# Optimization experiments

Measured on AMD Instinct MI355X. Metric: run time of the kernel, lower is better.

Reference implementation:

```python
import jax, jax.numpy as jnp
import numpy as np

B, N, F_IN = 8, 2048, 16
E, H = 64, 4
D = E // H
HID, A = 128, 4
QUEUE_IDX = np.array([0, 1, 2, 3, 6, 7, 8, 9, 10, 11, 12, 13])


def setup_inputs() -> dict:
    key = jax.random.key(0)
    ks = iter(jax.random.split(key, 64))
    def g(*s, scale=0.05):
        return jax.random.normal(next(ks), s, jnp.float32) * scale
    inp = {}
    inp['node_features'] = jax.random.normal(next(ks), (B, N, F_IN), jnp.float32) * 10.0
    inp['adjacency'] = jax.random.randint(next(ks), (B, N, N), 0, 2).astype(jnp.float32)
    for i, fin in enumerate([F_IN, E]):
        inp[f'l{i}_wq'] = g(fin, E)
        inp[f'l{i}_wk'] = g(fin, E)
        inp[f'l{i}_wv'] = g(fin, E)
        inp[f'l{i}_in_w'] = g(E, 3 * E)
        inp[f'l{i}_in_b'] = jnp.zeros(3 * E, jnp.float32)
        inp[f'l{i}_mha_ow'] = g(E, E)
        inp[f'l{i}_mha_ob'] = jnp.zeros(E, jnp.float32)
        inp[f'l{i}_op_w'] = g(E, E)
        inp[f'l{i}_op_b'] = jnp.zeros(E, jnp.float32)
    inp['head_w1'] = g(E, HID)
    inp['head_b1'] = jnp.zeros(HID, jnp.float32)
    inp['head_w2'] = g(HID, HID)
    inp['head_b2'] = jnp.zeros(HID, jnp.float32)
    inp['head_w3'] = g(HID, A, scale=0.001)
    inp['head_b3'] = jnp.zeros(A, jnp.float32)
    return inp


def _gat_layer(x, mask, wq, wk, wv, in_w, in_b, mow, mob, opw, opb):
    # x: [B,N,Fin], mask: [B,N,N] bool (True = blocked)
    b, n, _ = x.shape
    q = x @ wq  # layer's own Q/K/V projections (bias-free)
    k = x @ wk
    v = x @ wv
    # nn.MultiheadAttention's internal in_proj (with bias)
    Q = q @ in_w[:, :E] + in_b[:E]
    K = k @ in_w[:, E:2 * E] + in_b[E:2 * E]
    V = v @ in_w[:, 2 * E:] + in_b[2 * E:]
    Qh = Q.reshape(b, n, H, D)
    Kh = K.reshape(b, n, H, D)
    Vh = V.reshape(b, n, H, D)
    s = jnp.einsum('bqhd,bkhd->bhqk', Qh, Kh) / jnp.sqrt(jnp.float32(D))
    s = jnp.where(mask[:, None, :, :], -jnp.inf, s)
    a = jax.nn.softmax(s, axis=-1)  # diagonal always unmasked -> no all-inf rows
    o = jnp.einsum('bhqk,bkhd->bqhd', a, Vh).reshape(b, n, E)
    o = o @ mow + mob  # MHA out_proj
    return o @ opw + opb  # layer out_proj


def reference(node_features, adjacency,
              l0_wq, l0_wk, l0_wv, l0_in_w, l0_in_b, l0_mha_ow, l0_mha_ob, l0_op_w, l0_op_b,
              l1_wq, l1_wk, l1_wv, l1_in_w, l1_in_b, l1_mha_ow, l1_mha_ob, l1_op_w, l1_op_b,
              head_w1, head_b1, head_w2, head_b2, head_w3, head_b3):
    f = node_features.shape[-1]
    scale = jnp.ones(f, node_features.dtype).at[QUEUE_IDX].set(1.0 / 50.0).at[5].set(1.0 / 300.0)
    x = node_features * scale
    n = adjacency.shape[-1]
    mask = (adjacency + jnp.eye(n, dtype=adjacency.dtype)) == 0
    x = jax.nn.relu(_gat_layer(x, mask, l0_wq, l0_wk, l0_wv, l0_in_w, l0_in_b, l0_mha_ow, l0_mha_ob, l0_op_w, l0_op_b))
    x = jax.nn.relu(_gat_layer(x, mask, l1_wq, l1_wk, l1_wv, l1_in_w, l1_in_b, l1_mha_ow, l1_mha_ob, l1_op_w, l1_op_b))
    h = jax.nn.relu(x @ head_w1 + head_b1)
    h = jax.nn.relu(h @ head_w2 + head_b2)
    return h @ head_w3 + head_b3  # [B, N, n_actions]
```

## Files before the change

kernel.cpp:

```cpp
#include <hip/hip_runtime.h>

#define BB 8
#define NN 2048
#define FIN0 16
#define EE 64
#define HH 4
#define DD 16
#define HIDN 128
#define AA 4

__global__ __launch_bounds__(256) void k_mask(const float* __restrict__ adj, unsigned long long* __restrict__ mbT) {
    const int ITER = 32;
    for (int it = 0; it < ITER; it++) {
        long long idx = ((long long)blockIdx.x * ITER + it) * 256 + threadIdx.x;
        int k = (int)(idx & (NN - 1));
        int r = (int)((idx >> 11) & (NN - 1));
        int b = (int)(idx >> 22);
        float a = adj[idx];
        bool blocked = (a == 0.0f) && (k != r);
        unsigned long long m = __ballot(blocked);
        if ((threadIdx.x & 63) == 0) mbT[((long long)b * 32 + (k >> 6)) * NN + r] = m;
    }
}

#define QSCALE 0.36067376022224085f
__device__ __forceinline__ float sfeat(int f) {
    return (f == 4 || f == 14 || f == 15) ? 1.0f : ((f == 5) ? (1.0f / 300.0f) : 0.02f);
}
__global__ __launch_bounds__(256) void k_wcomb(
        const float* __restrict__ wq0, const float* __restrict__ wk0, const float* __restrict__ wv0,
        const float* __restrict__ inw0, const float* __restrict__ inb0,
        const float* __restrict__ mow0, const float* __restrict__ mob0,
        const float* __restrict__ opw0, const float* __restrict__ opb0,
        const float* __restrict__ wq1, const float* __restrict__ wk1, const float* __restrict__ wv1,
        const float* __restrict__ inw1, const float* __restrict__ inb1,
        const float* __restrict__ mow1, const float* __restrict__ mob1,
        const float* __restrict__ opw1, const float* __restrict__ opb1,
        float* __restrict__ CW0, float* __restrict__ WO0, float* __restrict__ bO0, float* __restrict__ bQ0,
        float* __restrict__ CW1, float* __restrict__ WO1, float* __restrict__ bO1, float* __restrict__ bQ1) {
    int ly = blockIdx.y;
    int fin = ly ? EE : FIN0;
    const float* wq = ly ? wq1 : wq0; const float* wk = ly ? wk1 : wk0; const float* wv = ly ? wv1 : wv0;
    const float* inw = ly ? inw1 : inw0; const float* inb = ly ? inb1 : inb0;
    const float* mow = ly ? mow1 : mow0; const float* mob = ly ? mob1 : mob0;
    const float* opw = ly ? opw1 : opw0; const float* opb = ly ? opb1 : opb0;
    float* CW = ly ? CW1 : CW0; float* WO = ly ? WO1 : WO0;
    float* bO = ly ? bO1 : bO0; float* bQ = ly ? bQ1 : bQ0;

    int t = blockIdx.x * 256 + threadIdx.x;
    int t1 = fin * 192;
    int t2 = t1 + 4096;
    int t3 = t2 + 64;
    int t4 = t3 + 192;
    if (t < t1) {
        int f = t / 192, j = t % 192;
        const float* w = (j < 64) ? wq : ((j < 128) ? wk : wv);
        float acc = 0.f;
        for (int kk = 0; kk < 64; kk++) acc += w[f * 64 + kk] * inw[kk * 192 + j];
        if (j < 64) acc *= QSCALE;
        if (ly == 0) acc *= sfeat(f);
        CW[t] = acc;
    } else if (t < t2) {
        int u = t - t1; int i = u >> 6, j = u & 63;
        float acc = 0.f;
        for (int kk = 0; kk < 64; kk++) acc += mow[i * 64 + kk] * opw[kk * 64 + j];
        WO[u] = acc;
    } else if (t < t3) {
        int j = t - t2;
        float acc = opb[j];
        for (int kk = 0; kk < 64; kk++) acc += mob[kk] * opw[kk * 64 + j];
        bO[j] = acc;
    } else if (t < t4) {
        int j = t - t3;
        bQ[j] = inb[j] * ((j < 64) ? QSCALE : 1.0f);
    }
}

template <int FINP>
__global__ __launch_bounds__(256) void k_qkv(const float* __restrict__ X, const float* __restrict__ CW,
                                             const float* __restrict__ bQ,
                                             float* __restrict__ Q, float* __restrict__ K, float* __restrict__ V) {
    int lane = threadIdx.x & 63;
    int quarter = threadIdx.x >> 6;
    int row = blockIdx.x * 64 + lane;
    int b = row >> 11, n = row & (NN - 1);
    float xr[FINP];
    const float4* xp = (const float4*)(X + (long long)row * FINP);
#pragma unroll
    for (int i = 0; i < FINP / 4; i++) {
        float4 v = xp[i];
        xr[4 * i] = v.x; xr[4 * i + 1] = v.y; xr[4 * i + 2] = v.z; xr[4 * i + 3] = v.w;
    }
    for (int jq = 0; jq < 12; jq++) {
        int j = quarter * 48 + jq * 4;
        float4 acc = *(const float4*)(bQ + j);
#pragma unroll
        for (int f = 0; f < FINP; f++) {
            float4 w = *(const float4*)(CW + f * 192 + j);
            acc.x = fmaf(xr[f], w.x, acc.x);
            acc.y = fmaf(xr[f], w.y, acc.y);
            acc.z = fmaf(xr[f], w.z, acc.z);
            acc.w = fmaf(xr[f], w.w, acc.w);
        }
        int which = j >> 6, c = j & 63, h = c >> 4, d = c & 15;
        float* dst = (which == 0) ? Q : ((which == 1) ? K : V);
        *(float4*)(dst + (((long long)(b * HH + h) * NN + n) * DD + d)) = acc;
    }
}

__global__ __launch_bounds__(256) void k_attn(const float* __restrict__ Q, const float* __restrict__ K,
                                              const float* __restrict__ V,
                                              const unsigned long long* __restrict__ mbT,
                                              float* __restrict__ O) {
    __shared__ __align__(16) float smem[2 * 4 * 64 * 17];
    int lane = threadIdx.x & 63;
    int w = threadIdx.x >> 6;
    int qb = blockIdx.x, h = blockIdx.y, b = blockIdx.z;
    int q0 = qb * 128 + lane;
    const float* Qp0 = Q + ((long long)((b * HH + h) * NN) + q0) * DD;
    const float4* qv0 = (const float4*)Qp0;
    const float4* qv1 = (const float4*)(Qp0 + 64 * DD);
    float4 q00 = qv0[0], q01 = qv0[1], q02 = qv0[2], q03 = qv0[3];
    float4 q10 = qv1[0], q11 = qv1[1], q12 = qv1[2], q13 = qv1[3];
    const float* Kb = K + (long long)(b * HH + h) * NN * DD;
    const float* Vb = V + (long long)(b * HH + h) * NN * DD;
    const unsigned long long* mrow = mbT + (long long)b * 32 * NN;
    float4 o00 = {0,0,0,0}, o01 = {0,0,0,0}, o02 = {0,0,0,0}, o03 = {0,0,0,0};
    float4 o10 = {0,0,0,0}, o11 = {0,0,0,0}, o12 = {0,0,0,0}, o13 = {0,0,0,0};
    float l0 = 0.f, l1 = 0.f;
    float* sK = smem + w * 2048;
    float* sV = sK + 1024;
    for (int c = 0; c < 8; c++) {
        int kc = w * 512 + c * 64;
        __syncthreads();
        const float4* srcK = (const float4*)(Kb + (long long)kc * DD);
        const float4* srcV = (const float4*)(Vb + (long long)kc * DD);
#pragma unroll
        for (int i = 0; i < 4; i++) {
            ((float4*)sK)[lane + 64 * i] = srcK[lane + 64 * i];
            ((float4*)sV)[lane + 64 * i] = srcV[lane + 64 * i];
        }
        unsigned long long mw0 = mrow[(long long)(kc >> 6) * NN + q0];
        unsigned long long mw1 = mrow[(long long)(kc >> 6) * NN + q0 + 64];
        __syncthreads();
#pragma unroll 4
        for (int kk = 0; kk < 64; kk++) {
            const float4* kr = (const float4*)(sK + kk * 16);
            float4 k0 = kr[0], k1 = kr[1], k2 = kr[2], k3 = kr[3];
            float cA = q00.x * k0.x;
            cA = fmaf(q00.y, k0.y, cA); cA = fmaf(q00.z, k0.z, cA); cA = fmaf(q00.w, k0.w, cA);
            cA = fmaf(q01.x, k1.x, cA); cA = fmaf(q01.y, k1.y, cA); cA = fmaf(q01.z, k1.z, cA); cA = fmaf(q01.w, k1.w, cA);
            float cB = q02.x * k2.x;
            cB = fmaf(q02.y, k2.y, cB); cB = fmaf(q02.z, k2.z, cB); cB = fmaf(q02.w, k2.w, cB);
            cB = fmaf(q03.x, k3.x, cB); cB = fmaf(q03.y, k3.y, cB); cB = fmaf(q03.w, k3.w, cB); cB = fmaf(q03.z, k3.z, cB);
            float cC = q10.x * k0.x;
            cC = fmaf(q10.y, k0.y, cC); cC = fmaf(q10.z, k0.z, cC); cC = fmaf(q10.w, k0.w, cC);
            cC = fmaf(q11.x, k1.x, cC); cC = fmaf(q11.y, k1.y, cC); cC = fmaf(q11.z, k1.z, cC); cC = fmaf(q11.w, k1.w, cC);
            float cD = q12.x * k2.x;
            cD = fmaf(q12.y, k2.y, cD); cD = fmaf(q12.z, k2.z, cD); cD = fmaf(q12.w, k2.w, cD);
            cD = fmaf(q13.x, k3.x, cD); cD = fmaf(q13.y, k3.y, cD); cD = fmaf(q13.z, k3.z, cD); cD = fmaf(q13.w, k3.w, cD);
            float e0 = __builtin_amdgcn_exp2f(cA + cB);
            float e1 = __builtin_amdgcn_exp2f(cC + cD);
            if ((mw0 >> kk) & 1ULL) e0 = 0.f;
            if ((mw1 >> kk) & 1ULL) e1 = 0.f;
            l0 += e0; l1 += e1;
            const float4* vr = (const float4*)(sV + kk * 16);
            float4 v0 = vr[0], v1 = vr[1], v2 = vr[2], v3 = vr[3];
            o00.x = fmaf(e0, v0.x, o00.x); o00.y = fmaf(e0, v0.y, o00.y); o00.z = fmaf(e0, v0.z, o00.z); o00.w = fmaf(e0, v0.w, o00.w);
            o01.x = fmaf(e0, v1.x, o01.x); o01.y = fmaf(e0, v1.y, o01.y); o01.z = fmaf(e0, v1.z, o01.z); o01.w = fmaf(e0, v1.w, o01.w);
            o02.x = fmaf(e0, v2.x, o02.x); o02.y = fmaf(e0, v2.y, o02.y); o02.z = fmaf(e0, v2.z, o02.z); o02.w = fmaf(e0, v2.w, o02.w);
            o03.x = fmaf(e0, v3.x, o03.x); o03.y = fmaf(e0, v3.y, o03.y); o03.z = fmaf(e0, v3.z, o03.z); o03.w = fmaf(e0, v3.w, o03.w);
            o10.x = fmaf(e1, v0.x, o10.x); o10.y = fmaf(e1, v0.y, o10.y); o10.z = fmaf(e1, v0.z, o10.z); o10.w = fmaf(e1, v0.w, o10.w);
            o11.x = fmaf(e1, v1.x, o11.x); o11.y = fmaf(e1, v1.y, o11.y); o11.z = fmaf(e1, v1.z, o11.z); o11.w = fmaf(e1, v1.w, o11.w);
            o12.x = fmaf(e1, v2.x, o12.x); o12.y = fmaf(e1, v2.y, o12.y); o12.z = fmaf(e1, v2.z, o12.z); o12.w = fmaf(e1, v2.w, o12.w);
            o13.x = fmaf(e1, v3.x, o13.x); o13.y = fmaf(e1, v3.y, o13.y); o13.z = fmaf(e1, v3.z, o13.z); o13.w = fmaf(e1, v3.w, o13.w);
        }
    }
    __syncthreads();
    {
        float* r0 = smem + (((0 * 4 + w) * 64 + lane)) * 17;
        r0[0]=o00.x; r0[1]=o00.y; r0[2]=o00.z; r0[3]=o00.w;
        r0[4]=o01.x; r0[5]=o01.y; r0[6]=o01.z; r0[7]=o01.w;
        r0[8]=o02.x; r0[9]=o02.y; r0[10]=o02.z; r0[11]=o02.w;
        r0[12]=o03.x; r0[13]=o03.y; r0[14]=o03.z; r0[15]=o03.w;
        r0[16]=l0;
        float* r1 = smem + (((1 * 4 + w) * 64 + lane)) * 17;
        r1[0]=o10.x; r1[1]=o10.y; r1[2]=o10.z; r1[3]=o10.w;
        r1[4]=o11.x; r1[5]=o11.y; r1[6]=o11.z; r1[7]=o11.w;
        r1[8]=o12.x; r1[9]=o12.y; r1[10]=o12.z; r1[11]=o12.w;
        r1[12]=o13.x; r1[13]=o13.y; r1[14]=o13.z; r1[15]=o13.w;
        r1[16]=l1;
    }
    __syncthreads();
    if (w < 2) {
        const float* basep = smem + ((w * 4) * 64 + lane) * 17;
        float acc[DD]; float lt = 0.f;
#pragma unroll
        for (int d = 0; d < DD; d++) acc[d] = 0.f;
#pragma unroll
        for (int s2 = 0; s2 < 4; s2++) {
            const float* pp = basep + s2 * 64 * 17;
#pragma unroll
            for (int d = 0; d < DD; d++) acc[d] += pp[d];
            lt += pp[16];
        }
        float inv = 1.0f / lt;
        int q = qb * 128 + w * 64 + lane;
        float* op = O + (long long)(b * NN + q) * EE + h * DD;
        float4 r0 = {acc[0]*inv, acc[1]*inv, acc[2]*inv, acc[3]*inv};
        float4 r1 = {acc[4]*inv, acc[5]*inv, acc[6]*inv, acc[7]*inv};
        float4 r2 = {acc[8]*inv, acc[9]*inv, acc[10]*inv, acc[11]*inv};
        float4 r3 = {acc[12]*inv, acc[13]*inv, acc[14]*inv, acc[15]*inv};
        ((float4*)op)[0] = r0; ((float4*)op)[1] = r1; ((float4*)op)[2] = r2; ((float4*)op)[3] = r3;
    }
}

__global__ __launch_bounds__(256) void k_out(const float* __restrict__ X, const float* __restrict__ WO,
                                             const float* __restrict__ bO, float* __restrict__ Y) {
    int lane = threadIdx.x & 63, quarter = threadIdx.x >> 6;
    long long row = (long long)blockIdx.x * 64 + lane;
    float xr[64];
    const float4* xp = (const float4*)(X + row * 64);
#pragma unroll
    for (int i = 0; i < 16; i++) {
        float4 t = xp[i];
        xr[4 * i] = t.x; xr[4 * i + 1] = t.y; xr[4 * i + 2] = t.z; xr[4 * i + 3] = t.w;
    }
    for (int jq = 0; jq < 4; jq++) {
        int j = quarter * 16 + jq * 4;
        float4 acc = *(const float4*)(bO + j);
#pragma unroll
        for (int f = 0; f < 64; f++) {
            float4 w4 = *(const float4*)(WO + f * 64 + j);
            acc.x = fmaf(xr[f], w4.x, acc.x);
            acc.y = fmaf(xr[f], w4.y, acc.y);
            acc.z = fmaf(xr[f], w4.z, acc.z);
            acc.w = fmaf(xr[f], w4.w, acc.w);
        }
        acc.x = fmaxf(acc.x, 0.f); acc.y = fmaxf(acc.y, 0.f);
        acc.z = fmaxf(acc.z, 0.f); acc.w = fmaxf(acc.w, 0.f);
        *(float4*)(Y + row * 64 + j) = acc;
    }
}

__global__ __launch_bounds__(128) void k_head(const float* __restrict__ X,
                                              const float* __restrict__ w1, const float* __restrict__ b1,
                                              const float* __restrict__ w2, const float* __restrict__ b2,
                                              const float* __restrict__ w3, const float* __restrict__ b3,
                                              float* __restrict__ out) {
    __shared__ float Xs[16 * 64];
    __shared__ float H1[16 * 128];
    __shared__ float H2[16 * 128];
    int tid = threadIdx.x;
    long long row0 = (long long)blockIdx.x * 16;
    {
        const float4* src = (const float4*)(X + row0 * 64);
        float4* dst = (float4*)Xs;
        dst[tid] = src[tid];
        dst[tid + 128] = src[tid + 128];
    }
    __syncthreads();
    {
        float wr[64];
#pragma unroll
        for (int f = 0; f < 64; f++) wr[f] = w1[f * 128 + tid];
        float bb = b1[tid];
        for (int r = 0; r < 16; r++) {
            const float4* x4 = (const float4*)(Xs + r * 64);
            float a0 = bb, a1 = 0.f, a2 = 0.f, a3 = 0.f;
#pragma unroll
            for (int fq = 0; fq < 16; fq++) {
                float4 xv = x4[fq];
                a0 = fmaf(xv.x, wr[4 * fq], a0);
                a1 = fmaf(xv.y, wr[4 * fq + 1], a1);
                a2 = fmaf(xv.z, wr[4 * fq + 2], a2);
                a3 = fmaf(xv.w, wr[4 * fq + 3], a3);
            }
            H1[r * 128 + tid] = fmaxf((a0 + a1) + (a2 + a3), 0.f);
        }
    }
    __syncthreads();
    {
        float wr2[128];
#pragma unroll
        for (int f = 0; f < 128; f++) wr2[f] = w2[f * 128 + tid];
        float bb2 = b2[tid];
        for (int r = 0; r < 16; r++) {
            const float4* h4 = (const float4*)(H1 + r * 128);
            float a0 = bb2, a1 = 0.f, a2 = 0.f, a3 = 0.f;
#pragma unroll
            for (int fq = 0; fq < 32; fq++) {
                float4 xv = h4[fq];
                a0 = fmaf(xv.x, wr2[4 * fq], a0);
                a1 = fmaf(xv.y, wr2[4 * fq + 1], a1);
                a2 = fmaf(xv.z, wr2[4 * fq + 2], a2);
                a3 = fmaf(xv.w, wr2[4 * fq + 3], a3);
            }
            H2[r * 128 + tid] = fmaxf((a0 + a1) + (a2 + a3), 0.f);
        }
    }
    __syncthreads();
    if (tid < 64) {
        int r = tid >> 2, a = tid & 3;
        float acc = b3[a];
        for (int f = 0; f < 128; f++) acc = fmaf(H2[r * 128 + f], w3[f * 4 + a], acc);
        out[(row0 + r) * 4 + a] = acc;
    }
}

extern "C" void kernel_launch(void* const* d_in, const int* in_sizes, int n_in,
                              void* d_out, int out_size, void* d_ws, size_t ws_size,
                              hipStream_t stream) {
    const float* nf = (const float*)d_in[0];
    const float* adj = (const float*)d_in[1];
    const float* l0[9]; for (int i = 0; i < 9; i++) l0[i] = (const float*)d_in[2 + i];
    const float* l1[9]; for (int i = 0; i < 9; i++) l1[i] = (const float*)d_in[11 + i];
    const float* hw1 = (const float*)d_in[20]; const float* hb1 = (const float*)d_in[21];
    const float* hw2 = (const float*)d_in[22]; const float* hb2 = (const float*)d_in[23];
    const float* hw3 = (const float*)d_in[24]; const float* hb3 = (const float*)d_in[25];
    float* out = (float*)d_out;

    char* ws = (char*)d_ws;
    size_t off = 0;
    auto alloc = [&](size_t bytes) -> void* {
        void* p = ws + off;
        off = (off + bytes + 255) & ~(size_t)255;
        return p;
    };
    unsigned long long* mbT = (unsigned long long*)alloc((size_t)BB * NN * NN / 8);
    float* Q = (float*)alloc((size_t)BB * HH * NN * DD * 4);
    float* K = (float*)alloc((size_t)BB * HH * NN * DD * 4);
    float* V = (float*)alloc((size_t)BB * HH * NN * DD * 4);
    float* O = (float*)alloc((size_t)BB * NN * EE * 4);
    float* x1 = (float*)alloc((size_t)BB * NN * EE * 4);
    float* x2 = (float*)alloc((size_t)BB * NN * EE * 4);
    float* CW0 = (float*)alloc(16 * 192 * 4);
    float* CW1 = (float*)alloc(64 * 192 * 4);
    float* WO0 = (float*)alloc(64 * 64 * 4);
    float* WO1 = (float*)alloc(64 * 64 * 4);
    float* bO0 = (float*)alloc(64 * 4);
    float* bO1 = (float*)alloc(64 * 4);
    float* bQ0 = (float*)alloc(192 * 4);
    float* bQ1 = (float*)alloc(192 * 4);

    k_mask<<<4096, 256, 0, stream>>>(adj, mbT);
    k_wcomb<<<dim3(65, 2), 256, 0, stream>>>(
        l0[0], l0[1], l0[2], l0[3], l0[4], l0[5], l0[6], l0[7], l0[8],
        l1[0], l1[1], l1[2], l1[3], l1[4], l1[5], l1[6], l1[7], l1[8],
        CW0, WO0, bO0, bQ0, CW1, WO1, bO1, bQ1);

    k_qkv<16><<<BB * NN / 64, 256, 0, stream>>>(nf, CW0, bQ0, Q, K, V);
    k_attn<<<dim3(NN / 128, HH, BB), 256, 0, stream>>>(Q, K, V, mbT, O);
    k_out<<<BB * NN / 64, 256, 0, stream>>>(O, WO0, bO0, x1);
    k_qkv<64><<<BB * NN / 64, 256, 0, stream>>>(x1, CW1, bQ1, Q, K, V);
    k_attn<<<dim3(NN / 128, HH, BB), 256, 0, stream>>>(Q, K, V, mbT, O);
    k_out<<<BB * NN / 64, 256, 0, stream>>>(O, WO1, bO1, x2);
    k_head<<<BB * NN / 16, 128, 0, stream>>>(x2, hw1, hb1, hw2, hb2, hw3, hb3, out);
}
```

Before: 705.1 us.

## Retile attention to four query rows per lane and fuse out-proj with QKV

The attention kernel now uses 512-thread blocks. Each lane holds four query rows instead of two, so every K/V row read from shared memory feeds twice as many score and accumulate FMAs. Each wave keeps a private K/V staging area, so the per-chunk block barriers are replaced by an LDS waitcnt, and the final reduction now sums eight wave partials. Separately, the layer-0 output projection and the layer-1 QKV projection are fused into one kernel that keeps the intermediate activations in shared memory, which drops a global round-trip and a launch. The risks are higher register pressure, a large shared-memory footprint that limits occupancy to one block per CU, and only 256 attention blocks for the whole grid.

```diff
diff --git a/kernel.cpp b/kernel.cpp
--- a/kernel.cpp
+++ b/kernel.cpp
@@ -108,31 +108,40 @@
     }
 }
 
-__global__ __launch_bounds__(256) void k_attn(const float* __restrict__ Q, const float* __restrict__ K,
-                                              const float* __restrict__ V,
-                                              const unsigned long long* __restrict__ mbT,
-                                              float* __restrict__ O) {
-    __shared__ __align__(16) float smem[2 * 4 * 64 * 17];
+__global__ __launch_bounds__(512, 2) void k_attn(const float* __restrict__ Q, const float* __restrict__ K,
+                                                 const float* __restrict__ V,
+                                                 const unsigned long long* __restrict__ mbT,
+                                                 float* __restrict__ O) {
+    __shared__ float smem[8 * 4 * 64 * 17];
     int lane = threadIdx.x & 63;
     int w = threadIdx.x >> 6;
     int qb = blockIdx.x, h = blockIdx.y, b = blockIdx.z;
-    int q0 = qb * 128 + lane;
-    const float* Qp0 = Q + ((long long)((b * HH + h) * NN) + q0) * DD;
-    const float4* qv0 = (const float4*)Qp0;
-    const float4* qv1 = (const float4*)(Qp0 + 64 * DD);
-    float4 q00 = qv0[0], q01 = qv0[1], q02 = qv0[2], q03 = qv0[3];
-    float4 q10 = qv1[0], q11 = qv1[1], q12 = qv1[2], q13 = qv1[3];
-    const float* Kb = K + (long long)(b * HH + h) * NN * DD;
-    const float* Vb = V + (long long)(b * HH + h) * NN * DD;
+    int qbase = qb * 256;
+
+    const float* Qbh = Q + (long long)(b * HH + h) * NN * DD;
+    const float* Kb  = K + (long long)(b * HH + h) * NN * DD;
+    const float* Vb  = V + (long long)(b * HH + h) * NN * DD;
     const unsigned long long* mrow = mbT + (long long)b * 32 * NN;
-    float4 o00 = {0,0,0,0}, o01 = {0,0,0,0}, o02 = {0,0,0,0}, o03 = {0,0,0,0};
-    float4 o10 = {0,0,0,0}, o11 = {0,0,0,0}, o12 = {0,0,0,0}, o13 = {0,0,0,0};
-    float l0 = 0.f, l1 = 0.f;
+
+    float4 qf[4][4];
+#pragma unroll
+    for (int rq = 0; rq < 4; rq++) {
+        const float4* qp = (const float4*)(Qbh + (long long)(qbase + rq * 64 + lane) * DD);
+#pragma unroll
+        for (int j = 0; j < 4; j++) qf[rq][j] = qp[j];
+    }
+    float4 oacc[4][4];
+#pragma unroll
+    for (int rq = 0; rq < 4; rq++)
+#pragma unroll
+        for (int j = 0; j < 4; j++) oacc[rq][j] = make_float4(0.f, 0.f, 0.f, 0.f);
+    float lsum[4] = {0.f, 0.f, 0.f, 0.f};
+
     float* sK = smem + w * 2048;
     float* sV = sK + 1024;
-    for (int c = 0; c < 8; c++) {
-        int kc = w * 512 + c * 64;
-        __syncthreads();
+
+    for (int c = 0; c < 4; c++) {
+        int kc = w * 256 + c * 64;
         const float4* srcK = (const float4*)(Kb + (long long)kc * DD);
         const float4* srcV = (const float4*)(Vb + (long long)kc * DD);
 #pragma unroll
@@ -140,72 +149,71 @@
             ((float4*)sK)[lane + 64 * i] = srcK[lane + 64 * i];
             ((float4*)sV)[lane + 64 * i] = srcV[lane + 64 * i];
         }
-        unsigned long long mw0 = mrow[(long long)(kc >> 6) * NN + q0];
-        unsigned long long mw1 = mrow[(long long)(kc >> 6) * NN + q0 + 64];
-        __syncthreads();
+        unsigned long long mw[4];
+        int kblk = w * 4 + c;
+#pragma unroll
+        for (int rq = 0; rq < 4; rq++) mw[rq] = mrow[(long long)kblk * NN + qbase + rq * 64 + lane];
+        asm volatile("s_waitcnt lgkmcnt(0)" ::: "memory");
 #pragma unroll 4
         for (int kk = 0; kk < 64; kk++) {
             const float4* kr = (const float4*)(sK + kk * 16);
             float4 k0 = kr[0], k1 = kr[1], k2 = kr[2], k3 = kr[3];
-            float cA = q00.x * k0.x;
-            cA = fmaf(q00.y, k0.y, cA); cA = fmaf(q00.z, k0.z, cA); cA = fmaf(q00.w, k0.w, cA);
-            cA = fmaf(q01.x, k1.x, cA); cA = fmaf(q01.y, k1.y, cA); cA = fmaf(q01.z, k1.z, cA); cA = fmaf(q01.w, k1.w, cA);
-            float cB = q02.x * k2.x;
-            cB = fmaf(q02.y, k2.y, cB); cB = fmaf(q02.z, k2.z, cB); cB = fmaf(q02.w, k2.w, cB);
-            cB = fmaf(q03.x, k3.x, cB); cB = fmaf(q03.y, k3.y, cB); cB = fmaf(q03.w, k3.w, cB); cB = fmaf(q03.z, k3.z, cB);
-            float cC = q10.x * k0.x;
-            cC = fmaf(q10.y, k0.y, cC); cC = fmaf(q10.z, k0.z, cC); cC = fmaf(q10.w, k0.w, cC);
-            cC = fmaf(q11.x, k1.x, cC); cC = fmaf(q11.y, k1.y, cC); cC = fmaf(q11.z, k1.z, cC); cC = fmaf(q11.w, k1.w, cC);
-            float cD = q12.x * k2.x;
-            cD = fmaf(q12.y, k2.y, cD); cD = fmaf(q12.z, k2.z, cD); cD = fmaf(q12.w, k2.w, cD);
-            cD = fmaf(q13.x, k3.x, cD); cD = fmaf(q13.y, k3.y, cD); cD = fmaf(q13.z, k3.z, cD); cD = fmaf(q13.w, k3.w, cD);
-            float e0 = __builtin_amdgcn_exp2f(cA + cB);
-            float e1 = __builtin_amdgcn_exp2f(cC + cD);
-            if ((mw0 >> kk) & 1ULL) e0 = 0.f;
-            if ((mw1 >> kk) & 1ULL) e1 = 0.f;
-            l0 += e0; l1 += e1;
+            float e[4];
+#pragma unroll
+            for (int rq = 0; rq < 4; rq++) {
+                float4 a0 = qf[rq][0], a1 = qf[rq][1], a2 = qf[rq][2], a3 = qf[rq][3];
+                float sA = a0.x * k0.x;
+                sA = fmaf(a0.y, k0.y, sA); sA = fmaf(a0.z, k0.z, sA); sA = fmaf(a0.w, k0.w, sA);
+                sA = fmaf(a1.x, k1.x, sA); sA = fmaf(a1.y, k1.y, sA); sA = fmaf(a1.z, k1.z, sA); sA = fmaf(a1.w, k1.w, sA);
+                float sB = a2.x * k2.x;
+                sB = fmaf(a2.y, k2.y, sB); sB = fmaf(a2.z, k2.z, sB); sB = fmaf(a2.w, k2.w, sB);
+                sB = fmaf(a3.x, k3.x, sB); sB = fmaf(a3.y, k3.y, sB); sB = fmaf(a3.z, k3.z, sB); sB = fmaf(a3.w, k3.w, sB);
+                float ee = __builtin_amdgcn_exp2f(sA + sB);
+                e[rq] = ((mw[rq] >> kk) & 1ULL) ? 0.f : ee;
+                lsum[rq] += e[rq];
+            }
             const float4* vr = (const float4*)(sV + kk * 16);
             float4 v0 = vr[0], v1 = vr[1], v2 = vr[2], v3 = vr[3];
-            o00.x = fmaf(e0, v0.x, o00.x); o00.y = fmaf(e0, v0.y, o00.y); o00.z = fmaf(e0, v0.z, o00.z); o00.w = fmaf(e0, v0.w, o00.w);
-            o01.x = fmaf(e0, v1.x, o01.x); o01.y = fmaf(e0, v1.y, o01.y); o01.z = fmaf(e0, v1.z, o01.z); o01.w = fmaf(e0, v1.w, o01.w);
-            o02.x = fmaf(e0, v2.x, o02.x); o02.y = fmaf(e0, v2.y, o02.y); o02.z = fmaf(e0, v2.z, o02.z); o02.w = fmaf(e0, v2.w, o02.w);
-            o03.x = fmaf(e0, v3.x, o03.x); o03.y = fmaf(e0, v3.y, o03.y); o03.z = fmaf(e0, v3.z, o03.z); o03.w = fmaf(e0, v3.w, o03.w);
-            o10.x = fmaf(e1, v0.x, o10.x); o10.y = fmaf(e1, v0.y, o10.y); o10.z = fmaf(e1, v0.z, o10.z); o10.w = fmaf(e1, v0.w, o10.w);
-            o11.x = fmaf(e1, v1.x, o11.x); o11.y = fmaf(e1, v1.y, o11.y); o11.z = fmaf(e1, v1.z, o11.z); o11.w = fmaf(e1, v1.w, o11.w);
-            o12.x = fmaf(e1, v2.x, o12.x); o12.y = fmaf(e1, v2.y, o12.y); o12.z = fmaf(e1, v2.z, o12.z); o12.w = fmaf(e1, v2.w, o12.w);
-            o13.x = fmaf(e1, v3.x, o13.x); o13.y = fmaf(e1, v3.y, o13.y); o13.z = fmaf(e1, v3.z, o13.z); o13.w = fmaf(e1, v3.w, o13.w);
-        }
-    }
-    __syncthreads();
-    {
-        float* r0 = smem + (((0 * 4 + w) * 64 + lane)) * 17;
-        r0[0]=o00.x; r0[1]=o00.y; r0[2]=o00.z; r0[3]=o00.w;
-        r0[4]=o01.x; r0[5]=o01.y; r0[6]=o01.z; r0[7]=o01.w;
-        r0[8]=o02.x; r0[9]=o02.y; r0[10]=o02.z; r0[11]=o02.w;
-        r0[12]=o03.x; r0[13]=o03.y; r0[14]=o03.z; r0[15]=o03.w;
-        r0[16]=l0;
-        float* r1 = smem + (((1 * 4 + w) * 64 + lane)) * 17;
-        r1[0]=o10.x; r1[1]=o10.y; r1[2]=o10.z; r1[3]=o10.w;
-        r1[4]=o11.x; r1[5]=o11.y; r1[6]=o11.z; r1[7]=o11.w;
-        r1[8]=o12.x; r1[9]=o12.y; r1[10]=o12.z; r1[11]=o12.w;
-        r1[12]=o13.x; r1[13]=o13.y; r1[14]=o13.z; r1[15]=o13.w;
-        r1[16]=l1;
-    }
-    __syncthreads();
-    if (w < 2) {
-        const float* basep = smem + ((w * 4) * 64 + lane) * 17;
+#pragma unroll
+            for (int rq = 0; rq < 4; rq++) {
+                float ew = e[rq];
+                oacc[rq][0].x = fmaf(ew, v0.x, oacc[rq][0].x); oacc[rq][0].y = fmaf(ew, v0.y, oacc[rq][0].y);
+                oacc[rq][0].z = fmaf(ew, v0.z, oacc[rq][0].z); oacc[rq][0].w = fmaf(ew, v0.w, oacc[rq][0].w);
+                oacc[rq][1].x = fmaf(ew, v1.x, oacc[rq][1].x); oacc[rq][1].y = fmaf(ew, v1.y, oacc[rq][1].y);
+                oacc[rq][1].z = fmaf(ew, v1.z, oacc[rq][1].z); oacc[rq][1].w = fmaf(ew, v1.w, oacc[rq][1].w);
+                oacc[rq][2].x = fmaf(ew, v2.x, oacc[rq][2].x); oacc[rq][2].y = fmaf(ew, v2.y, oacc[rq][2].y);
+                oacc[rq][2].z = fmaf(ew, v2.z, oacc[rq][2].z); oacc[rq][2].w = fmaf(ew, v2.w, oacc[rq][2].w);
+                oacc[rq][3].x = fmaf(ew, v3.x, oacc[rq][3].x); oacc[rq][3].y = fmaf(ew, v3.y, oacc[rq][3].y);
+                oacc[rq][3].z = fmaf(ew, v3.z, oacc[rq][3].z); oacc[rq][3].w = fmaf(ew, v3.w, oacc[rq][3].w);
+            }
+        }
+    }
+    __syncthreads();
+#pragma unroll
+    for (int rq = 0; rq < 4; rq++) {
+        float* rp = smem + (((w * 4 + rq) * 64 + lane)) * 17;
+#pragma unroll
+        for (int j = 0; j < 4; j++) {
+            rp[4 * j + 0] = oacc[rq][j].x; rp[4 * j + 1] = oacc[rq][j].y;
+            rp[4 * j + 2] = oacc[rq][j].z; rp[4 * j + 3] = oacc[rq][j].w;
+        }
+        rp[16] = lsum[rq];
+    }
+    __syncthreads();
+    if (w < 4) {
+        int rq = w;
         float acc[DD]; float lt = 0.f;
 #pragma unroll
         for (int d = 0; d < DD; d++) acc[d] = 0.f;
 #pragma unroll
-        for (int s2 = 0; s2 < 4; s2++) {
-            const float* pp = basep + s2 * 64 * 17;
+        for (int p = 0; p < 8; p++) {
+            const float* pp = smem + (((p * 4 + rq) * 64 + lane)) * 17;
 #pragma unroll
             for (int d = 0; d < DD; d++) acc[d] += pp[d];
             lt += pp[16];
         }
         float inv = 1.0f / lt;
-        int q = qb * 128 + w * 64 + lane;
+        int q = qbase + rq * 64 + lane;
         float* op = O + (long long)(b * NN + q) * EE + h * DD;
         float4 r0 = {acc[0]*inv, acc[1]*inv, acc[2]*inv, acc[3]*inv};
         float4 r1 = {acc[4]*inv, acc[5]*inv, acc[6]*inv, acc[7]*inv};
@@ -240,6 +248,65 @@
         acc.x = fmaxf(acc.x, 0.f); acc.y = fmaxf(acc.y, 0.f);
         acc.z = fmaxf(acc.z, 0.f); acc.w = fmaxf(acc.w, 0.f);
         *(float4*)(Y + row * 64 + j) = acc;
+    }
+}
+
+__global__ __launch_bounds__(256) void k_outqkv(const float* __restrict__ O, const float* __restrict__ WO,
+                                                const float* __restrict__ bO,
+                                                const float* __restrict__ CW, const float* __restrict__ bQ,
+                                                float* __restrict__ Q, float* __restrict__ K, float* __restrict__ V) {
+    __shared__ float xs[64 * 68];
+    int lane = threadIdx.x & 63, quarter = threadIdx.x >> 6;
+    long long row = (long long)blockIdx.x * 64 + lane;
+    int b = (int)(row >> 11), n = (int)(row & (NN - 1));
+    {
+        float xr[64];
+        const float4* xp = (const float4*)(O + row * 64);
+#pragma unroll
+        for (int i = 0; i < 16; i++) {
+            float4 t = xp[i];
+            xr[4 * i] = t.x; xr[4 * i + 1] = t.y; xr[4 * i + 2] = t.z; xr[4 * i + 3] = t.w;
+        }
+        for (int jq = 0; jq < 4; jq++) {
+            int j = quarter * 16 + jq * 4;
+            float4 acc = *(const float4*)(bO + j);
+#pragma unroll
+            for (int f = 0; f < 64; f++) {
+                float4 w4 = *(const float4*)(WO + f * 64 + j);
+                acc.x = fmaf(xr[f], w4.x, acc.x);
+                acc.y = fmaf(xr[f], w4.y, acc.y);
+                acc.z = fmaf(xr[f], w4.z, acc.z);
+                acc.w = fmaf(xr[f], w4.w, acc.w);
+            }
+            acc.x = fmaxf(acc.x, 0.f); acc.y = fmaxf(acc.y, 0.f);
+            acc.z = fmaxf(acc.z, 0.f); acc.w = fmaxf(acc.w, 0.f);
+            *(float4*)(xs + lane * 68 + j) = acc;
+        }
+    }
+    __syncthreads();
+    {
+        float xr[64];
+        const float4* xp = (const float4*)(xs + lane * 68);
+#pragma unroll
+        for (int i = 0; i < 16; i++) {
+            float4 t = xp[i];
+            xr[4 * i] = t.x; xr[4 * i + 1] = t.y; xr[4 * i + 2] = t.z; xr[4 * i + 3] = t.w;
+        }
+        for (int jq = 0; jq < 12; jq++) {
+            int j = quarter * 48 + jq * 4;
+            float4 acc = *(const float4*)(bQ + j);
+#pragma unroll
+            for (int f = 0; f < 64; f++) {
+                float4 w4 = *(const float4*)(CW + f * 192 + j);
+                acc.x = fmaf(xr[f], w4.x, acc.x);
+                acc.y = fmaf(xr[f], w4.y, acc.y);
+                acc.z = fmaf(xr[f], w4.z, acc.z);
+                acc.w = fmaf(xr[f], w4.w, acc.w);
+            }
+            int which = j >> 6, c = j & 63, h = c >> 4, d = c & 15;
+            float* dst = (which == 0) ? Q : ((which == 1) ? K : V);
+            *(float4*)(dst + (((long long)(b * HH + h) * NN + n) * DD + d)) = acc;
+        }
     }
 }
 
@@ -332,7 +399,6 @@
     float* K = (float*)alloc((size_t)BB * HH * NN * DD * 4);
     float* V = (float*)alloc((size_t)BB * HH * NN * DD * 4);
     float* O = (float*)alloc((size_t)BB * NN * EE * 4);
-    float* x1 = (float*)alloc((size_t)BB * NN * EE * 4);
     float* x2 = (float*)alloc((size_t)BB * NN * EE * 4);
     float* CW0 = (float*)alloc(16 * 192 * 4);
     float* CW1 = (float*)alloc(64 * 192 * 4);
@@ -350,10 +416,9 @@
         CW0, WO0, bO0, bQ0, CW1, WO1, bO1, bQ1);
 
     k_qkv<16><<<BB * NN / 64, 256, 0, stream>>>(nf, CW0, bQ0, Q, K, V);
-    k_attn<<<dim3(NN / 128, HH, BB), 256, 0, stream>>>(Q, K, V, mbT, O);
-    k_out<<<BB * NN / 64, 256, 0, stream>>>(O, WO0, bO0, x1);
-    k_qkv<64><<<BB * NN / 64, 256, 0, stream>>>(x1, CW1, bQ1, Q, K, V);
-    k_attn<<<dim3(NN / 128, HH, BB), 256, 0, stream>>>(Q, K, V, mbT, O);
+    k_attn<<<dim3(NN / 256, HH, BB), 512, 0, stream>>>(Q, K, V, mbT, O);
+    k_outqkv<<<BB * NN / 64, 256, 0, stream>>>(O, WO0, bO0, CW1, bQ1, Q, K, V);
+    k_attn<<<dim3(NN / 256, HH, BB), 512, 0, stream>>>(Q, K, V, mbT, O);
     k_out<<<BB * NN / 64, 256, 0, stream>>>(O, WO1, bO1, x2);
     k_head<<<BB * NN / 16, 128, 0, stream>>>(x2, hw1, hb1, hw2, hb2, hw3, hb3, out);
 }
```

Measured after the change: 639.2 us. 1.1x faster.
